# Kernel optimization log

Hardware: AMD Instinct MI355X
Metric: run time of the kernel (lower is better)

The kernel has to match this reference:

```python
import jax, jax.numpy as jnp
import numpy as np

N_NODES = 50000
N_EDGES = 800000
N_FEAT = 128
HIDDEN = 64
N_CLASSES = 16


def setup_inputs() -> dict:
    key = jax.random.key(0)
    ks = jax.random.split(key, 8)
    x = jax.random.normal(ks[0], (N_NODES, N_FEAT), dtype=jnp.float32)
    edge_index = jax.random.randint(ks[1], (2, N_EDGES), 0, N_NODES, dtype=jnp.int64)
    # GCNConv weights (glorot-like) and biases
    W1 = jax.random.normal(ks[2], (N_FEAT, HIDDEN), dtype=jnp.float32) / np.sqrt(N_FEAT)
    b1 = jnp.zeros((HIDDEN,), dtype=jnp.float32)
    W2 = jax.random.normal(ks[3], (HIDDEN, HIDDEN), dtype=jnp.float32) / np.sqrt(HIDDEN)
    b2 = jnp.zeros((HIDDEN,), dtype=jnp.float32)
    Wout = jax.random.normal(ks[4], (HIDDEN, N_CLASSES), dtype=jnp.float32) / np.sqrt(HIDDEN)
    bout = jnp.zeros((N_CLASSES,), dtype=jnp.float32)
    return {"x": x, "edge_index": edge_index, "W1": W1, "b1": b1,
            "W2": W2, "b2": b2, "Wout": Wout, "bout": bout}


def _gcn_conv(h, src, dst, norm, W, b, n_nodes):
    # h: [N, F_in]; linear transform then normalized scatter-add aggregation
    h = h @ W                                   # [N, F_out]
    msg = h[src] * norm[:, None]                # gather + scale  [E+N, F_out]
    out = jax.ops.segment_sum(msg, dst, num_segments=n_nodes)  # scatter-add
    return out + b


def reference(x, edge_index, W1, b1, W2, b2, Wout, bout):
    n = x.shape[0]
    # add self-loops (PyG GCNConv default add_self_loops=True)
    loops = jnp.arange(n, dtype=edge_index.dtype)
    src = jnp.concatenate([edge_index[0], loops])
    dst = jnp.concatenate([edge_index[1], loops])
    # symmetric normalization: deg^-1/2[src] * deg^-1/2[dst] (edge_weight = 1)
    ones = jnp.ones(src.shape[0], dtype=x.dtype)
    deg = jax.ops.segment_sum(ones, dst, num_segments=n)
    dinv = jnp.where(deg > 0, jax.lax.rsqrt(jnp.maximum(deg, 1e-12)), 0.0)
    norm = dinv[src] * dinv[dst]

    h = _gcn_conv(x, src, dst, norm, W1, b1, n)
    h = jax.nn.relu(h)
    # dropout p=0.5 with training=False -> identity
    h = _gcn_conv(h, src, dst, norm, W2, b2, n)
    h = jax.nn.relu(h)
    logits = h @ Wout + bout
    return jax.nn.softmax(logits, axis=1)
```

## Files before the change

kernel.cpp:

```cpp
#include <hip/hip_runtime.h>
#include <hip/hip_fp16.h>

#define N_NODES 50000
#define N_EDGES 800000
#define N_FEAT 128
#define HIDDEN 64
#define N_CLASSES 16
#define NBLK_NODE 196
#define TCAP 8192

__global__ void k_init(int* __restrict__ tileCur) {
    int tid = threadIdx.x;
    if (tid < NBLK_NODE) tileCur[tid] = tid * TCAP;
}

__global__ __launch_bounds__(256) void k_part(const int* __restrict__ ei,
                                              int* __restrict__ tileCur,
                                              int* __restrict__ binned) {
    __shared__ int cnt[NBLK_NODE], base[NBLK_NODE], cur[NBLK_NODE];
    int tid = threadIdx.x;
    int start = blockIdx.x * 4096;
    if (tid < NBLK_NODE) cnt[tid] = 0;
    __syncthreads();
    int s[16], d[16];
#pragma unroll
    for (int u = 0; u < 4; ++u) {
        int e0 = start + u * 1024 + tid * 4;
        if (e0 + 4 <= N_EDGES) {
            int4 s4 = *(const int4*)&ei[e0];
            int4 d4 = *(const int4*)&ei[N_EDGES + e0];
            s[u * 4 + 0] = s4.x; s[u * 4 + 1] = s4.y; s[u * 4 + 2] = s4.z; s[u * 4 + 3] = s4.w;
            d[u * 4 + 0] = d4.x; d[u * 4 + 1] = d4.y; d[u * 4 + 2] = d4.z; d[u * 4 + 3] = d4.w;
#pragma unroll
            for (int q = 0; q < 4; ++q) atomicAdd(&cnt[d[u * 4 + q] >> 8], 1);
        } else {
#pragma unroll
            for (int q = 0; q < 4; ++q) {
                int e = e0 + q;
                if (e < N_EDGES) {
                    s[u * 4 + q] = ei[e];
                    d[u * 4 + q] = ei[N_EDGES + e];
                    atomicAdd(&cnt[d[u * 4 + q] >> 8], 1);
                } else s[u * 4 + q] = -1;
            }
        }
    }
    __syncthreads();
    if (tid < NBLK_NODE) {
        base[tid] = atomicAdd(&tileCur[tid], cnt[tid]);
        cur[tid] = 0;
    }
    __syncthreads();
#pragma unroll
    for (int u = 0; u < 16; ++u) {
        if (s[u] < 0) continue;
        int t = d[u] >> 8;
        int r = atomicAdd(&cur[t], 1);
        int p = base[t] + r;
        if (p < (t + 1) * TCAP)
            binned[p] = s[u] | ((d[u] & 255) << 16);
    }
}

__global__ __launch_bounds__(256) void k_finesort(const int* __restrict__ binned,
                                                  const int* __restrict__ tileCur,
                                                  int* __restrict__ csr,
                                                  int2* __restrict__ rse,
                                                  float* __restrict__ dinv) {
    __shared__ int stage[TCAP];
    __shared__ int sc[256];
    __shared__ int cnt256[256];
    __shared__ int nodeOff[256];
    int tid = threadIdx.x;
    int tb = blockIdx.x;
    int beg = tb * TCAP;
    int m = tileCur[tb] - beg;
    if (m > TCAP) m = TCAP;
    cnt256[tid] = 0;
    __syncthreads();
    const int4* b4 = (const int4*)(binned + beg);
    int nv = m >> 2;
    for (int i = tid; i < nv; i += 256) {
        int4 r = b4[i];
        atomicAdd(&cnt256[(r.x >> 16) & 255], 1);
        atomicAdd(&cnt256[(r.y >> 16) & 255], 1);
        atomicAdd(&cnt256[(r.z >> 16) & 255], 1);
        atomicAdd(&cnt256[(r.w >> 16) & 255], 1);
    }
    for (int i = (m & ~3) + tid; i < m; i += 256)
        atomicAdd(&cnt256[(binned[beg + i] >> 16) & 255], 1);
    __syncthreads();
    int myc = cnt256[tid];
    sc[tid] = myc;
    __syncthreads();
#pragma unroll
    for (int off = 1; off < 256; off <<= 1) {
        int t = (tid >= off) ? sc[tid - off] : 0;
        __syncthreads();
        sc[tid] += t;
        __syncthreads();
    }
    int off0 = sc[tid] - myc;
    nodeOff[tid] = off0;
    int gnode = tb * 256 + tid;
    if (gnode < N_NODES) {
        dinv[gnode] = rsqrtf((float)myc + 1.0f);
        rse[gnode] = make_int2(beg + off0, myc);
    }
    cnt256[tid] = 0;
    __syncthreads();
    for (int i = tid; i < nv; i += 256) {
        int4 r = b4[i];
        int rr;
        rr = atomicAdd(&cnt256[(r.x >> 16) & 255], 1); stage[nodeOff[(r.x >> 16) & 255] + rr] = r.x & 0xFFFF;
        rr = atomicAdd(&cnt256[(r.y >> 16) & 255], 1); stage[nodeOff[(r.y >> 16) & 255] + rr] = r.y & 0xFFFF;
        rr = atomicAdd(&cnt256[(r.z >> 16) & 255], 1); stage[nodeOff[(r.z >> 16) & 255] + rr] = r.z & 0xFFFF;
        rr = atomicAdd(&cnt256[(r.w >> 16) & 255], 1); stage[nodeOff[(r.w >> 16) & 255] + rr] = r.w & 0xFFFF;
    }
    for (int i = (m & ~3) + tid; i < m; i += 256) {
        int rec = binned[beg + i];
        int dl = (rec >> 16) & 255;
        int rr = atomicAdd(&cnt256[dl], 1);
        stage[nodeOff[dl] + rr] = rec & 0xFFFF;
    }
    __syncthreads();
    int4* c4 = (int4*)(csr + beg);
    for (int i = tid; i < nv; i += 256) c4[i] = ((const int4*)stage)[i];
    for (int i = (m & ~3) + tid; i < m; i += 256) csr[beg + i] = stage[i];
}

template <int K, typename TIn>
__global__ __launch_bounds__(256) void k_mm(const TIn* __restrict__ a,
                                            const float* __restrict__ w,
                                            const float* __restrict__ dinv,
                                            __half* __restrict__ out) {
    __shared__ __align__(16) float At[K * 68];
    __shared__ __align__(16) float Ws[K * HIDDEN];
    int tid = threadIdx.x;
    long nbase = (long)blockIdx.x * 64;

    for (int i = tid; i < K * 16; i += 256)
        *(float4*)&Ws[i * 4] = *(const float4*)&w[i * 4];
    for (int i = tid; i < K * 16; i += 256) {
        int node = (i * 4) / K;
        int k = (i * 4) % K;
        long gn = nbase + node;
        float4 v;
        if (gn < N_NODES) {
            if constexpr (sizeof(TIn) == 2) {
                __half2 p0 = *(const __half2*)&a[gn * K + k];
                __half2 p1 = *(const __half2*)&a[gn * K + k + 2];
                float2 f0 = __half22float2(p0), f1 = __half22float2(p1);
                v = make_float4(f0.x, f0.y, f1.x, f1.y);
            } else {
                v = *(const float4*)&a[gn * K + k];
            }
        } else v = make_float4(0.f, 0.f, 0.f, 0.f);
        At[(k + 0) * 68 + node] = v.x;
        At[(k + 1) * 68 + node] = v.y;
        At[(k + 2) * 68 + node] = v.z;
        At[(k + 3) * 68 + node] = v.w;
    }
    __syncthreads();

    int tx = tid & 15;
    int ty = tid >> 4;
    float acc[4][4] = {};
#pragma unroll 8
    for (int k = 0; k < K; ++k) {
        float av[4], wv[4];
        *(float4*)av = *(const float4*)&At[k * 68 + ty * 4];
        *(float4*)wv = *(const float4*)&Ws[k * HIDDEN + tx * 4];
#pragma unroll
        for (int i = 0; i < 4; ++i)
#pragma unroll
            for (int j = 0; j < 4; ++j)
                acc[i][j] = fmaf(av[i], wv[j], acc[i][j]);
    }
#pragma unroll
    for (int i = 0; i < 4; ++i) {
        long n = nbase + ty * 4 + i;
        if (n < N_NODES) {
            float di = dinv[n];
            __half2* op = (__half2*)&out[n * HIDDEN + tx * 4];
            op[0] = __floats2half2_rn(acc[i][0] * di, acc[i][1] * di);
            op[1] = __floats2half2_rn(acc[i][2] * di, acc[i][3] * di);
        }
    }
}

__device__ __forceinline__ void acc_row8(float* a, int4 rv) {
    float2 f;
    f = __half22float2(*(__half2*)&rv.x); a[0] += f.x; a[1] += f.y;
    f = __half22float2(*(__half2*)&rv.y); a[2] += f.x; a[3] += f.y;
    f = __half22float2(*(__half2*)&rv.z); a[4] += f.x; a[5] += f.y;
    f = __half22float2(*(__half2*)&rv.w); a[6] += f.x; a[7] += f.y;
}

__global__ void k_gather(const __half* __restrict__ h, const int* __restrict__ csr,
                         const int2* __restrict__ rse, const float* __restrict__ dinv,
                         const float* __restrict__ bias, __half* __restrict__ out) {
    int t = blockIdx.x * 256 + threadIdx.x;
    int node = __builtin_amdgcn_readfirstlane(t >> 6);
    int lane = t & 63;
    int e8 = lane >> 3;
    int q = lane & 7;
    int2 se = rse[node];
    int r0 = se.x, r1 = se.x + se.y;
    float dd = dinv[node];

    float a[8] = {0.f, 0.f, 0.f, 0.f, 0.f, 0.f, 0.f, 0.f};
    if (e8 == 0)
        acc_row8(a, *(const int4*)&h[(long)node * HIDDEN + q * 8]);

    int j = r0;
    while (j + 16 <= r1) {
        int sA = csr[j + e8];
        int sB = csr[j + 8 + e8];
        int4 rA = *(const int4*)&h[(long)sA * HIDDEN + q * 8];
        int4 rB = *(const int4*)&h[(long)sB * HIDDEN + q * 8];
        acc_row8(a, rA);
        acc_row8(a, rB);
        j += 16;
    }
    if (j + 8 <= r1) {
        int sA = csr[j + e8];
        acc_row8(a, *(const int4*)&h[(long)sA * HIDDEN + q * 8]);
        j += 8;
    }
    int rem = r1 - j;
    if (e8 < rem) {
        int sA = csr[j + e8];
        acc_row8(a, *(const int4*)&h[(long)sA * HIDDEN + q * 8]);
    }
#pragma unroll
    for (int off = 8; off < 64; off <<= 1)
#pragma unroll
        for (int i = 0; i < 8; ++i) a[i] += __shfl_xor(a[i], off, 64);

    if (e8 == 0) {
        float4 b0 = *(const float4*)&bias[q * 8];
        float4 b1 = *(const float4*)&bias[q * 8 + 4];
        float r[8];
        r[0] = fmaxf(fmaf(a[0], dd, b0.x), 0.f);
        r[1] = fmaxf(fmaf(a[1], dd, b0.y), 0.f);
        r[2] = fmaxf(fmaf(a[2], dd, b0.z), 0.f);
        r[3] = fmaxf(fmaf(a[3], dd, b0.w), 0.f);
        r[4] = fmaxf(fmaf(a[4], dd, b1.x), 0.f);
        r[5] = fmaxf(fmaf(a[5], dd, b1.y), 0.f);
        r[6] = fmaxf(fmaf(a[6], dd, b1.z), 0.f);
        r[7] = fmaxf(fmaf(a[7], dd, b1.w), 0.f);
        __half2 h0 = __floats2half2_rn(r[0], r[1]);
        __half2 h1 = __floats2half2_rn(r[2], r[3]);
        __half2 h2 = __floats2half2_rn(r[4], r[5]);
        __half2 h3 = __floats2half2_rn(r[6], r[7]);
        int4 o;
        o.x = *(int*)&h0; o.y = *(int*)&h1; o.z = *(int*)&h2; o.w = *(int*)&h3;
        *(int4*)&out[(long)node * HIDDEN + q * 8] = o;
    }
}

__global__ void k_out(const __half* __restrict__ h, const float* __restrict__ w,
                      const float* __restrict__ b, float* __restrict__ out) {
    __shared__ float Ws[HIDDEN * N_CLASSES];
    __shared__ float bs[N_CLASSES];
    int tid = threadIdx.x;
    for (int i = tid; i < HIDDEN * N_CLASSES; i += 256) Ws[i] = w[i];
    if (tid < N_CLASSES) bs[tid] = b[tid];
    __syncthreads();
    int node = blockIdx.x * 16 + (tid >> 4);
    int c = tid & 15;
    const __half* hr = h + (long)node * HIDDEN;
    float acc = bs[c];
#pragma unroll
    for (int k = 0; k < HIDDEN; ++k)
        acc = fmaf(__half2float(hr[k]), Ws[k * N_CLASSES + c], acc);
    float m = acc;
#pragma unroll
    for (int off = 8; off; off >>= 1) m = fmaxf(m, __shfl_xor(m, off, 16));
    float ex = expf(acc - m);
    float s = ex;
#pragma unroll
    for (int off = 8; off; off >>= 1) s += __shfl_xor(s, off, 16);
    out[(long)node * N_CLASSES + c] = ex / s;
}

extern "C" void kernel_launch(void* const* d_in, const int* in_sizes, int n_in,
                              void* d_out, int out_size, void* d_ws, size_t ws_size,
                              hipStream_t stream) {
    const float* x    = (const float*)d_in[0];
    const int*   ei   = (const int*)d_in[1];
    const float* W1   = (const float*)d_in[2];
    const float* b1   = (const float*)d_in[3];
    const float* W2   = (const float*)d_in[4];
    const float* b2   = (const float*)d_in[5];
    const float* Wout = (const float*)d_in[6];
    const float* bout = (const float*)d_in[7];
    float* out = (float*)d_out;

    char* ws = (char*)d_ws;
    int2*   rse     = (int2*)ws;                       ws += 400128;
    float*  dinv    = (float*)ws;                      ws += 200192;
    int*    tileCur = (int*)ws;                        ws += 1024;
    int*    csr     = (int*)ws;                        ws += (size_t)NBLK_NODE * TCAP * 4;
    char*   slotA   = ws;                              ws += 6553600;
    __half* bufB    = (__half*)ws;
    int*    binned  = (int*)slotA;
    __half* bufA    = (__half*)slotA;

    const int NB_MM = (N_NODES + 63) / 64;
    const int NB_E16 = (N_EDGES + 4095) / 4096;

    k_init<<<1, 256, 0, stream>>>(tileCur);
    k_part<<<NB_E16, 256, 0, stream>>>(ei, tileCur, binned);
    k_finesort<<<NBLK_NODE, 256, 0, stream>>>(binned, tileCur, csr, rse, dinv);

    k_mm<N_FEAT, float><<<NB_MM, 256, 0, stream>>>(x, W1, dinv, bufA);
    k_gather<<<N_NODES / 4, 256, 0, stream>>>(bufA, csr, rse, dinv, b1, bufB);

    k_mm<HIDDEN, __half><<<NB_MM, 256, 0, stream>>>(bufB, W2, dinv, bufA);
    k_gather<<<N_NODES / 4, 256, 0, stream>>>(bufA, csr, rse, dinv, b2, bufB);

    k_out<<<N_NODES / 16, 256, 0, stream>>>(bufB, Wout, bout, out);
}
```

Measured before the change: 187.4 us.

## Use MFMA f16 matrix cores for node feature transform GEMM

Replaces the scalar FMA register-tiled GEMM in k_mm with MFMA 16x16x32 f16 instructions. Inputs and weights are converted to half and stored in padded LDS, with the weights kept transposed. Each wave computes a 16x64 output tile. This cuts ALU time in the dense transform, but converts the fp32 input x to half before the multiply and writes outputs as scattered 2-byte stores.

Measured after the change: 171.5 us. -8.5%, faster.

```diff
diff --git a/kernel.cpp b/kernel.cpp
--- a/kernel.cpp
+++ b/kernel.cpp
@@ -8,6 +8,9 @@
 #define N_CLASSES 16
 #define NBLK_NODE 196
 #define TCAP 8192
+
+typedef _Float16 f16x8 __attribute__((ext_vector_type(8)));
+typedef float f32x4 __attribute__((ext_vector_type(4)));
 
 __global__ void k_init(int* __restrict__ tileCur) {
     int tid = threadIdx.x;
@@ -134,57 +137,72 @@
                                             const float* __restrict__ w,
                                             const float* __restrict__ dinv,
                                             __half* __restrict__ out) {
-    __shared__ __align__(16) float At[K * 68];
-    __shared__ __align__(16) float Ws[K * HIDDEN];
+    constexpr int LDK = K + 8;
+    __shared__ __align__(16) __half A_lds[64 * LDK];
+    __shared__ __align__(16) __half Wt_lds[64 * LDK];
     int tid = threadIdx.x;
     long nbase = (long)blockIdx.x * 64;
 
-    for (int i = tid; i < K * 16; i += 256)
-        *(float4*)&Ws[i * 4] = *(const float4*)&w[i * 4];
     for (int i = tid; i < K * 16; i += 256) {
-        int node = (i * 4) / K;
-        int k = (i * 4) % K;
-        long gn = nbase + node;
-        float4 v;
+        int k = (i * 4) >> 6;
+        int f0 = (i * 4) & 63;
+        float4 v = *(const float4*)&w[i * 4];
+        Wt_lds[(f0 + 0) * LDK + k] = __float2half(v.x);
+        Wt_lds[(f0 + 1) * LDK + k] = __float2half(v.y);
+        Wt_lds[(f0 + 2) * LDK + k] = __float2half(v.z);
+        Wt_lds[(f0 + 3) * LDK + k] = __float2half(v.w);
+    }
+    for (int i = tid; i < 64 * K / 8; i += 256) {
+        int n = (i * 8) / K;
+        int k0 = (i * 8) % K;
+        long gn = nbase + n;
+        if constexpr (sizeof(TIn) == 4) {
+            float4 v0, v1;
+            if (gn < N_NODES) {
+                v0 = *(const float4*)&a[gn * K + k0];
+                v1 = *(const float4*)&a[gn * K + k0 + 4];
+            } else {
+                v0 = make_float4(0.f, 0.f, 0.f, 0.f);
+                v1 = v0;
+            }
+            __half2* dst = (__half2*)&A_lds[n * LDK + k0];
+            dst[0] = __floats2half2_rn(v0.x, v0.y);
+            dst[1] = __floats2half2_rn(v0.z, v0.w);
+            dst[2] = __floats2half2_rn(v1.x, v1.y);
+            dst[3] = __floats2half2_rn(v1.z, v1.w);
+        } else {
+            int4 v = (gn < N_NODES) ? *(const int4*)&a[gn * K + k0]
+                                    : make_int4(0, 0, 0, 0);
+            *(int4*)&A_lds[n * LDK + k0] = v;
+        }
+    }
+    __syncthreads();
+
+    int wv = tid >> 6;
+    int lane = tid & 63;
+    int m = lane & 15;
+    int quad = lane >> 4;
+    const __half* Arow = &A_lds[(wv * 16 + m) * LDK + quad * 8];
+    f32x4 acc[4] = {};
+#pragma unroll
+    for (int t = 0; t < K; t += 32) {
+        f16x8 af = *(const f16x8*)(const void*)&Arow[t];
+#pragma unroll
+        for (int g = 0; g < 4; ++g) {
+            f16x8 bf = *(const f16x8*)(const void*)&Wt_lds[(g * 16 + m) * LDK + t + quad * 8];
+            acc[g] = __builtin_amdgcn_mfma_f32_16x16x32_f16(af, bf, acc[g], 0, 0, 0);
+        }
+    }
+
+#pragma unroll
+    for (int r = 0; r < 4; ++r) {
+        int n = wv * 16 + quad * 4 + r;
+        long gn = nbase + n;
         if (gn < N_NODES) {
-            if constexpr (sizeof(TIn) == 2) {
-                __half2 p0 = *(const __half2*)&a[gn * K + k];
-                __half2 p1 = *(const __half2*)&a[gn * K + k + 2];
-                float2 f0 = __half22float2(p0), f1 = __half22float2(p1);
-                v = make_float4(f0.x, f0.y, f1.x, f1.y);
-            } else {
-                v = *(const float4*)&a[gn * K + k];
-            }
-        } else v = make_float4(0.f, 0.f, 0.f, 0.f);
-        At[(k + 0) * 68 + node] = v.x;
-        At[(k + 1) * 68 + node] = v.y;
-        At[(k + 2) * 68 + node] = v.z;
-        At[(k + 3) * 68 + node] = v.w;
-    }
-    __syncthreads();
-
-    int tx = tid & 15;
-    int ty = tid >> 4;
-    float acc[4][4] = {};
-#pragma unroll 8
-    for (int k = 0; k < K; ++k) {
-        float av[4], wv[4];
-        *(float4*)av = *(const float4*)&At[k * 68 + ty * 4];
-        *(float4*)wv = *(const float4*)&Ws[k * HIDDEN + tx * 4];
-#pragma unroll
-        for (int i = 0; i < 4; ++i)
-#pragma unroll
-            for (int j = 0; j < 4; ++j)
-                acc[i][j] = fmaf(av[i], wv[j], acc[i][j]);
-    }
-#pragma unroll
-    for (int i = 0; i < 4; ++i) {
-        long n = nbase + ty * 4 + i;
-        if (n < N_NODES) {
-            float di = dinv[n];
-            __half2* op = (__half2*)&out[n * HIDDEN + tx * 4];
-            op[0] = __floats2half2_rn(acc[i][0] * di, acc[i][1] * di);
-            op[1] = __floats2half2_rn(acc[i][2] * di, acc[i][3] * di);
+            float di = dinv[gn];
+#pragma unroll
+            for (int g = 0; g < 4; ++g)
+                out[gn * HIDDEN + g * 16 + m] = __float2half(acc[g][r] * di);
         }
     }
 }
```
